# Optimization experiments

Measured on AMD Instinct MI355X. Metric: run time of the kernel, lower is better.

The kernel has to match this reference:

```python
import jax, jax.numpy as jnp
import numpy as np

N, S_CT, D = 64, 128, 1024
WIN = 5
EPS = 1e-8
STOP = 0.1
MAX_DEPTH = 25


def layer_norm(x, g, b, eps=1e-5):
    mu = jnp.mean(x, axis=-1, keepdims=True)
    var = jnp.var(x, axis=-1, keepdims=True)
    return (x - mu) / jnp.sqrt(var + eps) * g + b


def _augment(sequence, input_mask, START, END):
    n, s, d = sequence.shape
    seq = jnp.concatenate([jnp.broadcast_to(START, (n, 1, d)), sequence], axis=1)
    m = jnp.concatenate([jnp.ones((n, 1, 1), seq.dtype), input_mask], axis=1)
    m_no_end = jnp.concatenate([m, jnp.zeros((n, 1, 1), seq.dtype)], axis=1)
    m_yes_end = jnp.concatenate([jnp.ones((n, 1, 1), seq.dtype), m], axis=1)
    end_mask = m_yes_end - m_no_end  # one-hot at END slot
    seq = jnp.concatenate([seq, jnp.zeros((n, 1, d), seq.dtype)], axis=1)
    seq = end_mask * END + (1.0 - end_mask) * seq
    m_no_start = jnp.concatenate([jnp.zeros((n, 1, 1), seq.dtype), m_yes_end[:, 1:]], axis=1)
    return seq, m_yes_end, end_mask, m_no_start, m_no_end


def _neighbor_probs(exist_probs, mask):
    # exist_probs, mask: (n,s,1). Returns left/right soft-neighbor matrices (n,s,s).
    n, s, _ = mask.shape
    m = jnp.stack([mask[:, ::-1, 0], mask[:, :, 0]], axis=1)            # (n,2,s)
    p = jnp.stack([exist_probs[:, ::-1, 0], exist_probs[:, :, 0]], axis=1)
    tri = jnp.triu(jnp.ones((s, s), mask.dtype), k=1)
    mat = (p * m)[:, :, None, :] * tri                                   # (n,2,s,s)
    cs = jnp.cumsum(mat, axis=-1)
    rem_left = jnp.concatenate([jnp.ones((n, 2, s, 1), mask.dtype), 1.0 - cs[..., :-1]], axis=-1)
    rem_left = jnp.maximum(rem_left, 0.0)
    right = jnp.where(cs > 1.0, rem_left, mat) * m[:, :, None, :]
    left = jnp.flip(right[:, 0], axis=(1, 2))
    return left, right[:, 1]


def crvnn_forward(sequence, input_mask, START, END, W_conv, b_conv, W_scorer, b_scorer,
                  W_init, b_init, W_cell1, b_cell1, W_cell2, b_cell2,
                  ln1_g, ln1_b, ln2_g, ln2_b):
    seq, mask, end_mask, m_no_start, m_no_end = _augment(sequence, input_mask, START, END)
    n, s, d = seq.shape
    last_mask = jnp.concatenate([end_mask[:, 1:], jnp.zeros((n, 1, 1), seq.dtype)], axis=1)
    sel_mask = m_no_start * m_no_end * (1.0 - last_mask)  # start_end_last_mask
    seq = layer_norm((seq * mask) @ W_init + b_init, ln1_g, ln1_b) * mask
    exist = jnp.ones((n, s, 1), seq.dtype) * mask

    def step(carry, _):
        sq, ep, um = carry
        L, R = _neighbor_probs(ep, mask)
        l1 = L @ sq; l2 = L @ l1
        r1 = R @ sq; r2 = R @ r1
        win = jnp.concatenate([l2, l1, sq, r1, r2], axis=-1)  # (n,s,5d) == stacked window flattened
        h = jax.nn.gelu(win @ W_conv + b_conv, approximate=False)
        sc = h @ W_scorer + b_scorer                           # (n,s,1) transition score
        scores = jnp.concatenate([sc, jnp.zeros_like(sc)], axis=-1)
        exp_scores = jnp.exp(scores - jnp.max(scores))
        exp_t = exp_scores[..., 0:1] * sel_mask
        exp_n = exp_scores[..., 1:2]
        # sum_normalize over {transition, no_op}; gate halted samples via um (tp=0 => no-op)
        tp = exp_t / (exp_t + exp_n + 2.0 * EPS) * um[:, None, None]
        # compose(left_child, self)
        cat = jnp.concatenate([l1, sq], axis=-1)
        hid = jax.nn.gelu(cat @ W_cell1 + b_cell1, approximate=False)
        contents = (hid @ W_cell2 + b_cell2).reshape(n, s, 4, d)
        gates = jax.nn.sigmoid(contents[:, :, 0:3, :])
        comp = layer_norm(gates[:, :, 0] * l1 + gates[:, :, 1] * sq + gates[:, :, 2] * contents[:, :, 3, :], ln2_g, ln2_b)
        new_sq = tp * comp + (1.0 - tp) * sq
        new_ep = ep * (1.0 - (R @ tp))  # left neighbor consumed with prob of right neighbor transition
        active = jnp.sum(new_ep * sel_mask, axis=(1, 2))
        new_um = um * (active >= STOP).astype(sq.dtype)
        return (new_sq, new_ep, new_um), None

    steps = min(s - 2, MAX_DEPTH)
    (seq, exist, _), _ = jax.lax.scan(step, (seq, exist, jnp.ones((n,), seq.dtype)), None, length=steps)
    seq = seq * mask
    global_state = jnp.sum(last_mask * seq, axis=1)  # root lands at last content slot
    return seq[:, 1:-1, :], global_state


def setup_inputs():
    key = jax.random.key(0)
    ks = jax.random.split(key, 8)
    sc = 0.02
    f32 = jnp.float32
    return {
        "sequence": jax.random.normal(ks[0], (N, S_CT, D), f32),
        "input_mask": jnp.ones((N, S_CT, 1), f32),
        "START": jax.random.normal(ks[1], (D,), f32),
        "END": jax.random.normal(ks[2], (D,), f32),
        "W_conv": jax.random.normal(ks[3], (WIN * D, D), f32) * sc,
        "b_conv": jnp.zeros((D,), f32),
        "W_scorer": jax.random.normal(ks[4], (D, 1), f32) * sc,
        "b_scorer": jnp.zeros((1,), f32),
        "W_init": jax.random.normal(ks[5], (D, D), f32) * sc,
        "b_init": jnp.zeros((D,), f32),
        "W_cell1": jax.random.normal(ks[6], (2 * D, 4 * D), f32) * sc,
        "b_cell1": jnp.zeros((4 * D,), f32),
        "W_cell2": jax.random.normal(ks[7], (4 * D, 4 * D), f32) * sc,
        "b_cell2": jnp.zeros((4 * D,), f32),
        "ln1_g": jnp.ones((D,), f32), "ln1_b": jnp.zeros((D,), f32),
        "ln2_g": jnp.ones((D,), f32), "ln2_b": jnp.zeros((D,), f32),
    }


def reference(sequence, input_mask, START, END, W_conv, b_conv, W_scorer, b_scorer,
              W_init, b_init, W_cell1, b_cell1, W_cell2, b_cell2,
              ln1_g, ln1_b, ln2_g, ln2_b):
    return crvnn_forward(sequence, input_mask, START, END, W_conv, b_conv, W_scorer, b_scorer,
                         W_init, b_init, W_cell1, b_cell1, W_cell2, b_cell2,
                         ln1_g, ln1_b, ln2_g, ln2_b)
```

## Files before the change

kernel.cpp:

```cpp
#include <hip/hip_runtime.h>
#include <math.h>


#define NB 64
#define SS 130
#define DD 1024
#define MM (NB*SS)
#define LSTR 132
#define CROWS 1664
#define RSC 2048.0f
#define IRS (1.0f/2048.0f)

typedef _Float16 f16x8 __attribute__((ext_vector_type(8)));
typedef _Float16 f16x4 __attribute__((ext_vector_type(4)));
typedef _Float16 f16x2 __attribute__((ext_vector_type(2)));
typedef float f32x4 __attribute__((ext_vector_type(4)));

struct GemmSrcF { const float* a[5]; };
struct GemmSrcP { const _Float16* h[5]; const _Float16* l[5]; };
struct hl2 { _Float16 h, l; };

__device__ __forceinline__ float bsum(float v){
  __shared__ float sh[4];
  __syncthreads();
  #pragma unroll
  for (int o=32;o;o>>=1) v += __shfl_down(v,o);
  if ((threadIdx.x & 63)==0) sh[threadIdx.x>>6] = v;
  __syncthreads();
  return sh[0]+sh[1]+sh[2]+sh[3];
}
__device__ __forceinline__ float bmaxr(float v){
  __shared__ float sh[4];
  __syncthreads();
  #pragma unroll
  for (int o=32;o;o>>=1) v = fmaxf(v,__shfl_down(v,o));
  if ((threadIdx.x & 63)==0) sh[threadIdx.x>>6] = v;
  __syncthreads();
  return fmaxf(fmaxf(sh[0],sh[1]),fmaxf(sh[2],sh[3]));
}
__device__ __forceinline__ float gelu_(float x){
  return 0.5f*x*(1.f+erff(x*0.70710678118654752f));
}
__device__ __forceinline__ hl2 enc(float x){
  hl2 r;
  r.h = (_Float16)x;
  r.l = (_Float16)((x - (float)r.h)*RSC);
  return r;
}

__global__ __launch_bounds__(256) void build_masks(
    const float* __restrict__ im, float* __restrict__ mk, float* __restrict__ sel,
    float* __restrict__ lastm, float* __restrict__ endm, float* __restrict__ ep,
    float* __restrict__ um, int* __restrict__ flag){
  int b = blockIdx.x, i = threadIdx.x;
  if (i < SS){
    float mye = (i<=1) ? 1.f : im[b*128 + (i-2)];
    float mne = (i==SS-1) ? 0.f : ((i==0) ? 1.f : im[b*128 + (i-1)]);
    float em  = mye - mne;
    float mns = (i==0) ? 0.f : mye;
    float lm;
    if (i < SS-1){
      int i1 = i+1;
      float mye1 = (i1<=1) ? 1.f : im[b*128 + (i1-2)];
      float mne1 = (i1==SS-1) ? 0.f : im[b*128 + (i1-1)];
      lm = mye1 - mne1;
    } else lm = 0.f;
    float sl = mns * mne * (1.f - lm);
    int idx = b*SS + i;
    mk[idx]=mye; sel[idx]=sl; lastm[idx]=lm; endm[idx]=em; ep[idx]=mye;
  } else if (i == SS) { um[b] = 1.f; }
  else if (i == SS+1 && b==0) { flag[0] = 0; }
}

__global__ __launch_bounds__(256) void build_seq(
    const float* __restrict__ seqin, const float* __restrict__ START,
    const float* __restrict__ END, const float* __restrict__ mk,
    const float* __restrict__ endm, float* __restrict__ out){
  int r = blockIdx.x; int b = r/SS, i = r%SS; int t = threadIdx.x;
  float em = endm[r], m = mk[r];
  #pragma unroll
  for (int q=0;q<4;q++){
    int j = t + q*256;
    float v;
    if (i==0) v = START[j];
    else if (i<=128) v = seqin[((size_t)b*128 + (i-1))*DD + j];
    else v = 0.f;
    v = em*END[j] + (1.f-em)*v;
    out[(size_t)r*DD + j] = v*m;
  }
}

__global__ __launch_bounds__(256) void wtranspose(
    const float* __restrict__ W, _Float16* __restrict__ WTh, _Float16* __restrict__ WTl,
    int K, int N){
  __shared__ float Ts[32][33];
  int k0 = blockIdx.x*32, n0 = blockIdx.y*32;
  int t = threadIdx.x;
  int r = t>>3, c4 = (t&7)*4;
  float4 v = *(const float4*)(W + (size_t)(k0+r)*N + n0 + c4);
  Ts[r][c4]=v.x; Ts[r][c4+1]=v.y; Ts[r][c4+2]=v.z; Ts[r][c4+3]=v.w;
  __syncthreads();
  int n = t>>3, k4 = (t&7)*4;
  f16x4 h, lo;
  #pragma unroll
  for (int i=0;i<4;i++){
    hl2 e = enc(Ts[k4+i][n] * 64.f);
    h[i] = e.h; lo[i] = e.l;
  }
  *(f16x4*)(WTh + (size_t)(n0+n)*K + k0+k4) = h;
  *(f16x4*)(WTl + (size_t)(n0+n)*K + k0+k4) = lo;
}

template<bool PREW>
__global__ __launch_bounds__(256,2) void gemm_mfma(
    GemmSrcP S, long lda,
    const _Float16* __restrict__ WTh, const _Float16* __restrict__ WTl,
    const float* __restrict__ Wf, int Nw,
    const float* __restrict__ bias,
    float* __restrict__ C, _Float16* __restrict__ Ch, _Float16* __restrict__ Cl,
    long ldc, int K, int act,
    const int* __restrict__ flag, float* __restrict__ spart, const float* __restrict__ Ws){
  if (flag[0]) return;
  __shared__ _Float16 Ah[128][40], Al[128][40];
  __shared__ _Float16 Wh[128][40], Wl[128][40];
  const int t = threadIdx.x;
  const int wave = t >> 6, lane = t & 63;
  const int wm = wave >> 1, wn = wave & 1;
  const int l15 = lane & 15, l4 = lane >> 4;
  int lin = blockIdx.y * gridDim.x + blockIdx.x;
  int nwg = gridDim.x * gridDim.y;
  int q = nwg >> 3, r = nwg & 7;
  int xcd = lin & 7, pos = lin >> 3;
  int wg = (xcd < r) ? (xcd*(q+1) + pos) : (r*(q+1) + (xcd - r)*q + pos);
  int MT = gridDim.y;
  int mt = wg % MT, nt = wg / MT;
  const long mb = (long)mt * 128;
  const int  nb = nt * 128;
  f32x4 accH[4][4], accX[4][4];
  #pragma unroll
  for (int i=0;i<4;i++)
    #pragma unroll
    for (int j=0;j<4;j++){ accH[i][j] = (f32x4){0.f,0.f,0.f,0.f}; accX[i][j] = (f32x4){0.f,0.f,0.f,0.f}; }

  for (int kt=0; kt<K; kt+=32){
    #pragma unroll
    for (int p=0;p<2;p++){
      int f = t + 256*p;
      int m = f >> 2;
      int ko = (f & 3) * 8;
      int kg = kt + ko;
      const _Float16* sh = S.h[kg >> 10];
      const _Float16* sl = S.l[kg >> 10];
      *(f16x8*)&Ah[m][ko] = *(const f16x8*)(sh + (mb + m)*lda + (kg & 1023));
      *(f16x8*)&Al[m][ko] = *(const f16x8*)(sl + (mb + m)*lda + (kg & 1023));
    }
    if constexpr (PREW){
      #pragma unroll
      for (int p=0;p<2;p++){
        int f = t + 256*p;
        int n = f >> 2;
        int ko = (f & 3) * 8;
        *(f16x8*)&Wh[n][ko] = *(const f16x8*)(WTh + (size_t)(nb + n)*K + kt + ko);
        *(f16x8*)&Wl[n][ko] = *(const f16x8*)(WTl + (size_t)(nb + n)*K + kt + ko);
      }
    } else {
      #pragma unroll
      for (int p=0;p<2;p++){
        int u = t + 256*p;
        int kp = u >> 5;
        int c  = u & 31;
        const float* wsrc = Wf + (size_t)(kt + 2*kp)*Nw + nb + c;
        #pragma unroll
        for (int i=0;i<4;i++){
          hl2 e0 = enc(wsrc[32*i] * 64.f);
          hl2 e1 = enc(wsrc[(size_t)Nw + 32*i] * 64.f);
          f16x2 hp; hp[0]=e0.h; hp[1]=e1.h;
          f16x2 lp; lp[0]=e0.l; lp[1]=e1.l;
          int n = c + 32*i;
          *(f16x2*)&Wh[n][2*kp] = hp;
          *(f16x2*)&Wl[n][2*kp] = lp;
        }
      }
    }
    __syncthreads();
    f16x8 wh[4], wl[4];
    #pragma unroll
    for (int i=0;i<4;i++){
      wh[i] = *(const f16x8*)&Wh[wn*64 + i*16 + l15][8*l4];
      wl[i] = *(const f16x8*)&Wl[wn*64 + i*16 + l15][8*l4];
    }
    #pragma unroll
    for (int mi=0;mi<4;mi++){
      f16x8 ahv = *(const f16x8*)&Ah[wm*64 + mi*16 + l15][8*l4];
      f16x8 alv = *(const f16x8*)&Al[wm*64 + mi*16 + l15][8*l4];
      #pragma unroll
      for (int ni=0;ni<4;ni++){
        accH[mi][ni] = __builtin_amdgcn_mfma_f32_16x16x32_f16(wh[ni], ahv, accH[mi][ni], 0,0,0);
        accX[mi][ni] = __builtin_amdgcn_mfma_f32_16x16x32_f16(wh[ni], alv, accX[mi][ni], 0,0,0);
        accX[mi][ni] = __builtin_amdgcn_mfma_f32_16x16x32_f16(wl[ni], ahv, accX[mi][ni], 0,0,0);
      }
    }
    __syncthreads();
  }

  const float IH = 1.f/64.f, IX = 1.f/131072.f;
  if (act==2){
    #pragma unroll
    for (int mi=0;mi<4;mi++){
      float s = 0.f;
      #pragma unroll
      for (int ni=0;ni<4;ni++){
        int nbase = nb + wn*64 + ni*16 + 4*l4;
        #pragma unroll
        for (int rr=0;rr<4;rr++){
          float v = gelu_(accH[mi][ni][rr]*IH + accX[mi][ni][rr]*IX + bias[nbase+rr]);
          s = fmaf(v, Ws[nbase+rr], s);
        }
      }
      s += __shfl_xor(s, 16);
      s += __shfl_xor(s, 32);
      if (l4==0){
        long m = mb + wm*64 + mi*16 + l15;
        spart[m*16 + nt*2 + wn] = s;
      }
    }
    return;
  }
  #pragma unroll
  for (int mi=0;mi<4;mi++){
    long m = mb + wm*64 + mi*16 + l15;
    #pragma unroll
    for (int ni=0;ni<4;ni++){
      int nbase = nb + wn*64 + ni*16 + 4*l4;
      float v0 = accH[mi][ni][0]*IH + accX[mi][ni][0]*IX + bias[nbase+0];
      float v1 = accH[mi][ni][1]*IH + accX[mi][ni][1]*IX + bias[nbase+1];
      float v2 = accH[mi][ni][2]*IH + accX[mi][ni][2]*IX + bias[nbase+2];
      float v3 = accH[mi][ni][3]*IH + accX[mi][ni][3]*IX + bias[nbase+3];
      if (act==1){
        v0=gelu_(v0); v1=gelu_(v1); v2=gelu_(v2); v3=gelu_(v3);
        hl2 e0=enc(v0), e1=enc(v1), e2=enc(v2), e3=enc(v3);
        f16x4 h4; h4[0]=e0.h; h4[1]=e1.h; h4[2]=e2.h; h4[3]=e3.h;
        f16x4 l4v; l4v[0]=e0.l; l4v[1]=e1.l; l4v[2]=e2.l; l4v[3]=e3.l;
        *(f16x4*)(Ch + m*ldc + nbase) = h4;
        *(f16x4*)(Cl + m*ldc + nbase) = l4v;
      } else {
        float4 v; v.x=v0; v.y=v1; v.z=v2; v.w=v3;
        *(float4*)(C + m*ldc + nbase) = v;
      }
    }
  }
}

__global__ __launch_bounds__(256,2) void gemm_f32(
    GemmSrcF S, long lda, const float* __restrict__ B, const float* __restrict__ bias,
    float* __restrict__ C, long ldc, int N, int K, int act,
    const int* __restrict__ flag){
  if (flag[0]) return;
  __shared__ float Asm[16][132];
  __shared__ float Bsm[16][132];
  float acc[8][8];
  #pragma unroll
  for (int i=0;i<8;i++)
    #pragma unroll
    for (int j=0;j<8;j++) acc[i][j]=0.f;
  const int t = threadIdx.x;
  const int tx = t & 15, ty = t >> 4;
  const long mb = (long)blockIdx.y * 128;
  const int  nb = blockIdx.x * 128;
  for (int kt=0; kt<K; kt+=16){
    #pragma unroll
    for (int ii=0; ii<2; ii++){
      int f  = t + 256*ii;
      int m  = f >> 2;
      int k4 = (f & 3) * 4;
      int kg = kt + k4;
      const float* src = S.a[kg >> 10];
      float4 v = *(const float4*)(src + (mb + m)*lda + (kg & 1023));
      Asm[k4+0][m]=v.x; Asm[k4+1][m]=v.y; Asm[k4+2][m]=v.z; Asm[k4+3][m]=v.w;
    }
    #pragma unroll
    for (int ii=0; ii<2; ii++){
      int f  = t + 256*ii;
      int kk = f >> 5;
      int c4 = (f & 31)*4;
      *(float4*)&Bsm[kk][c4] = *(const float4*)(B + (long)(kt+kk)*N + nb + c4);
    }
    __syncthreads();
    #pragma unroll
    for (int kk=0;kk<16;kk++){
      float av[8], bv[8];
      *(float4*)&av[0] = *(const float4*)&Asm[kk][ty*4];
      *(float4*)&av[4] = *(const float4*)&Asm[kk][64+ty*4];
      *(float4*)&bv[0] = *(const float4*)&Bsm[kk][tx*4];
      *(float4*)&bv[4] = *(const float4*)&Bsm[kk][64+tx*4];
      #pragma unroll
      for (int r=0;r<8;r++)
        #pragma unroll
        for (int c=0;c<8;c++) acc[r][c] = fmaf(av[r],bv[c],acc[r][c]);
    }
    __syncthreads();
  }
  #pragma unroll
  for (int rh=0;rh<2;rh++)
  #pragma unroll
  for (int rr=0;rr<4;rr++){
    long row = mb + rh*64 + ty*4 + rr;
    #pragma unroll
    for (int ch=0;ch<2;ch++){
      int col = nb + ch*64 + tx*4;
      float4 v;
      v.x = acc[rh*4+rr][ch*4+0] + bias[col+0];
      v.y = acc[rh*4+rr][ch*4+1] + bias[col+1];
      v.z = acc[rh*4+rr][ch*4+2] + bias[col+2];
      v.w = acc[rh*4+rr][ch*4+3] + bias[col+3];
      *(float4*)(C + row*ldc + col) = v;
    }
  }
}

__global__ __launch_bounds__(256,2) void bgemm(
    const float* __restrict__ P,
    const _Float16* __restrict__ Xh, const _Float16* __restrict__ Xl,
    _Float16* __restrict__ Yh, _Float16* __restrict__ Yl,
    const int* __restrict__ flag){
  if (flag[0]) return;
  __shared__ float Ps[64][17];
  __shared__ float Xs[16][132];
  const int t = threadIdx.x;
  const int nt = blockIdx.x, mt = blockIdx.y, b = blockIdx.z;
  const int i0 = mt*64;
  const float* Pb = P + (size_t)b*SS*LSTR;
  const _Float16* Xhb = Xh + (size_t)b*SS*DD + nt*128;
  const _Float16* Xlb = Xl + (size_t)b*SS*DD + nt*128;
  _Float16* Yhb = Yh + (size_t)b*SS*DD + nt*128;
  _Float16* Ylb = Yl + (size_t)b*SS*DD + nt*128;
  const int tx = t & 7, ty = t >> 3;
  float acc[2][16];
  #pragma unroll
  for (int r=0;r<2;r++)
    #pragma unroll
    for (int c=0;c<16;c++) acc[r][c]=0.f;
  for (int j0=0;j0<SS;j0+=16){
    { int r = t>>2, c0 = (t&3)*4;
      float4 v = make_float4(0.f,0.f,0.f,0.f);
      if (i0 + r < SS && j0 + c0 < LSTR) v = *(const float4*)(Pb + (size_t)(i0+r)*LSTR + j0 + c0);
      Ps[r][c0]=v.x; Ps[r][c0+1]=v.y; Ps[r][c0+2]=v.z; Ps[r][c0+3]=v.w;
    }
    #pragma unroll
    for (int ii=0;ii<2;ii++){
      int f = t + 256*ii;
      int jj = f>>5, c4 = (f&31)*4;
      float x0=0.f,x1=0.f,x2=0.f,x3=0.f;
      if (j0 + jj < SS){
        f16x4 xh = *(const f16x4*)(Xhb + (size_t)(j0+jj)*DD + c4);
        f16x4 xl = *(const f16x4*)(Xlb + (size_t)(j0+jj)*DD + c4);
        x0 = (float)xh[0] + (float)xl[0]*IRS;
        x1 = (float)xh[1] + (float)xl[1]*IRS;
        x2 = (float)xh[2] + (float)xl[2]*IRS;
        x3 = (float)xh[3] + (float)xl[3]*IRS;
      }
      Xs[jj][c4]=x0; Xs[jj][c4+1]=x1; Xs[jj][c4+2]=x2; Xs[jj][c4+3]=x3;
    }
    __syncthreads();
    #pragma unroll
    for (int jj=0;jj<16;jj++){
      float p0 = Ps[2*ty][jj], p1 = Ps[2*ty+1][jj];
      #pragma unroll
      for (int q=0;q<4;q++){
        float4 xv = *(const float4*)&Xs[jj][tx*4 + 32*q];
        acc[0][q*4+0] = fmaf(p0,xv.x,acc[0][q*4+0]);
        acc[0][q*4+1] = fmaf(p0,xv.y,acc[0][q*4+1]);
        acc[0][q*4+2] = fmaf(p0,xv.z,acc[0][q*4+2]);
        acc[0][q*4+3] = fmaf(p0,xv.w,acc[0][q*4+3]);
        acc[1][q*4+0] = fmaf(p1,xv.x,acc[1][q*4+0]);
        acc[1][q*4+1] = fmaf(p1,xv.y,acc[1][q*4+1]);
        acc[1][q*4+2] = fmaf(p1,xv.z,acc[1][q*4+2]);
        acc[1][q*4+3] = fmaf(p1,xv.w,acc[1][q*4+3]);
      }
    }
    __syncthreads();
  }
  #pragma unroll
  for (int rr=0;rr<2;rr++){
    int row = i0 + 2*ty + rr;
    if (row < SS){
      #pragma unroll
      for (int q=0;q<4;q++){
        hl2 e0 = enc(acc[rr][q*4+0]);
        hl2 e1 = enc(acc[rr][q*4+1]);
        hl2 e2 = enc(acc[rr][q*4+2]);
        hl2 e3 = enc(acc[rr][q*4+3]);
        f16x4 h4; h4[0]=e0.h; h4[1]=e1.h; h4[2]=e2.h; h4[3]=e3.h;
        f16x4 l4v; l4v[0]=e0.l; l4v[1]=e1.l; l4v[2]=e2.l; l4v[3]=e3.l;
        *(f16x4*)(Yhb + (size_t)row*DD + tx*4 + 32*q) = h4;
        *(f16x4*)(Ylb + (size_t)row*DD + tx*4 + 32*q) = l4v;
      }
    }
  }
}

__global__ __launch_bounds__(256) void neighbor_kernel(
    const float* __restrict__ ep, const float* __restrict__ mk,
    float* __restrict__ L, float* __restrict__ R, const int* __restrict__ flag){
  if (flag[0]) return;
  int wave = threadIdx.x >> 6, lane = threadIdx.x & 63;
  int idx = blockIdx.x*4 + wave;
  if (idx >= MM) return;
  int b = idx / SS, i = idx % SS;
  const float* p = ep + b*SS;
  const float* m = mk + b*SS;
  float mR[3], mL[3], mv[3];
  #pragma unroll
  for (int c=0;c<3;c++){
    int j = lane + 64*c;
    float pj = (j<SS)? p[j] : 0.f;
    float mj = (j<SS)? m[j] : 0.f;
    mv[c] = mj;
    float x = pj*mj;
    mR[c] = (j>i)? x : 0.f;
    mL[c] = (j<i)? x : 0.f;
  }
  float csR[3]; float run = 0.f;
  #pragma unroll
  for (int c=0;c<3;c++){
    float s = mR[c];
    #pragma unroll
    for (int o=1;o<64;o<<=1){ float v = __shfl_up(s,o); if (lane>=o) s += v; }
    csR[c] = s + run;
    run += __shfl(s,63);
  }
  float csL[3]; run = 0.f;
  #pragma unroll
  for (int cc=0;cc<3;cc++){
    int c = 2-cc;
    float s = mL[c];
    #pragma unroll
    for (int o=1;o<64;o<<=1){ float v = __shfl_down(s,o); if (lane < 64-o) s += v; }
    csL[c] = s + run;
    run += __shfl(s,0);
  }
  float* Lr = L + (size_t)idx*LSTR;
  float* Rr = R + (size_t)idx*LSTR;
  #pragma unroll
  for (int c=0;c<3;c++){
    int j = lane + 64*c;
    if (j < LSTR){
      float rv = 0.f, lv = 0.f;
      if (j < SS){
        rv = ((csR[c]>1.f) ? fmaxf(1.f-(csR[c]-mR[c]),0.f) : mR[c]) * mv[c];
        lv = ((csL[c]>1.f) ? fmaxf(1.f-(csL[c]-mL[c]),0.f) : mL[c]) * mv[c];
      }
      Rr[j] = rv; Lr[j] = lv;
    }
  }
}

__global__ __launch_bounds__(256) void ln1_kernel(
    const float* __restrict__ xin, const float* __restrict__ g, const float* __restrict__ bb,
    const float* __restrict__ mk, _Float16* __restrict__ sqh, _Float16* __restrict__ sql){
  int r = blockIdx.x, t = threadIdx.x;
  const float* xr = xin + (size_t)r*DD;
  float x[4]; float s=0.f;
  #pragma unroll
  for (int q=0;q<4;q++){ x[q]=xr[t+256*q]; s+=x[q]; }
  float mean = bsum(s)*(1.f/DD);
  float vs=0.f;
  #pragma unroll
  for (int q=0;q<4;q++){ float d=x[q]-mean; vs+=d*d; }
  float var = bsum(vs)*(1.f/DD);
  float inv = 1.f/sqrtf(var+1e-5f);
  float m = mk[r];
  #pragma unroll
  for (int q=0;q<4;q++){
    int j=t+256*q;
    float v = ((x[q]-mean)*inv*g[j]+bb[j])*m;
    hl2 e = enc(v);
    sqh[(size_t)r*DD+j] = e.h; sql[(size_t)r*DD+j] = e.l;
  }
}

__global__ void scorer_final(const float* __restrict__ spart, const float* __restrict__ bs,
                             float* __restrict__ sc, const int* __restrict__ flag){
  if (flag[0]) return;
  int r = blockIdx.x*blockDim.x + threadIdx.x;
  if (r >= MM) return;
  float s = bs[0];
  #pragma unroll
  for (int k=0;k<16;k++) s += spart[(size_t)r*16+k];
  sc[r] = s;
}
__global__ __launch_bounds__(256) void max1(const float* __restrict__ sc, float* __restrict__ part,
                                            const int* __restrict__ flag){
  if (flag[0]) return;
  int idx = blockIdx.x*256 + threadIdx.x;
  float v = -1e30f;
  for (int i = idx; i < MM; i += 64*256) v = fmaxf(v, sc[i]);
  v = bmaxr(v);
  if (threadIdx.x==0) part[blockIdx.x] = v;
}
__global__ __launch_bounds__(64) void max2(const float* __restrict__ part, float* __restrict__ gm,
                                           const int* __restrict__ flag){
  if (flag[0]) return;
  float v = part[threadIdx.x];
  #pragma unroll
  for (int o=32;o;o>>=1) v = fmaxf(v, __shfl_down(v,o));
  if (threadIdx.x==0) gm[0] = fmaxf(v, 0.f);
}
__global__ void tp_kernel(const float* __restrict__ sc, const float* __restrict__ sel,
                          const float* __restrict__ um, const float* __restrict__ gm,
                          float* __restrict__ tp, const int* __restrict__ flag){
  if (flag[0]) return;
  int idx = blockIdx.x*blockDim.x + threadIdx.x;
  if (idx>=MM) return;
  int b = idx / SS;
  float g = gm[0];
  float et = expf(sc[idx]-g)*sel[idx];
  float en = expf(-g);
  tp[idx] = et/(et+en+2e-8f)*um[b];
}

__global__ __launch_bounds__(256) void update_kernel(
    const float* __restrict__ cont,
    const _Float16* __restrict__ l1h, const _Float16* __restrict__ l1l,
    _Float16* __restrict__ sqh, _Float16* __restrict__ sql,
    const float* __restrict__ tp, const float* __restrict__ g, const float* __restrict__ bb,
    const int* __restrict__ flag, long row0){
  if (flag[0]) return;
  long r = row0 + blockIdx.x; int t = threadIdx.x;
  const float* cr = cont + (size_t)blockIdx.x*4096;
  const _Float16* lh = l1h + (size_t)r*DD;
  const _Float16* ll = l1l + (size_t)r*DD;
  _Float16* sh = sqh + (size_t)r*DD;
  _Float16* sl = sql + (size_t)r*DD;
  float x[4], sv[4];
  float s=0.f;
  #pragma unroll
  for (int q=0;q<4;q++){
    int j = t+q*256;
    float c0=cr[j], c1=cr[DD+j], c2=cr[2*DD+j], c3=cr[3*DD+j];
    float g0=1.f/(1.f+expf(-c0));
    float g1=1.f/(1.f+expf(-c1));
    float g2=1.f/(1.f+expf(-c2));
    float lv = (float)lh[j] + (float)ll[j]*IRS;
    float sqv = (float)sh[j] + (float)sl[j]*IRS;
    sv[q]=sqv;
    x[q] = g0*lv + g1*sqv + g2*c3;
    s += x[q];
  }
  float mean = bsum(s)*(1.f/DD);
  float vs=0.f;
  #pragma unroll
  for (int q=0;q<4;q++){ float d=x[q]-mean; vs+=d*d; }
  float var = bsum(vs)*(1.f/DD);
  float inv = 1.f/sqrtf(var+1e-5f);
  float tpv = tp[r];
  #pragma unroll
  for (int q=0;q<4;q++){
    int j=t+q*256;
    float comp = (x[q]-mean)*inv*g[j]+bb[j];
    float out = tpv*comp + (1.f-tpv)*sv[q];
    hl2 e = enc(out);
    sh[j]=e.h; sl[j]=e.l;
  }
}

__global__ __launch_bounds__(256) void ep_update(
    float* __restrict__ ep, const float* __restrict__ R,
    const float* __restrict__ tp, const int* __restrict__ flag){
  if (flag[0]) return;
  int wave = threadIdx.x >> 6, lane = threadIdx.x & 63;
  int idx = blockIdx.x*4 + wave;
  if (idx >= MM) return;
  int b = idx / SS;
  const float* Rr = R + (size_t)idx*LSTR;
  const float* tb = tp + b*SS;
  float d = 0.f;
  #pragma unroll
  for (int c=0;c<3;c++){
    int j = lane + 64*c;
    if (j < SS) d = fmaf(Rr[j], tb[j], d);
  }
  #pragma unroll
  for (int o=32;o;o>>=1) d += __shfl_xor(d,o);
  if (lane==0) ep[idx] *= (1.f - d);
}

__global__ __launch_bounds__(256) void active_um(const float* __restrict__ ep,
                                                 const float* __restrict__ sel,
                                                 float* __restrict__ um,
                                                 const int* __restrict__ flag){
  if (flag[0]) return;
  int b = blockIdx.x, t = threadIdx.x;
  float s = (t<SS) ? ep[b*SS+t]*sel[b*SS+t] : 0.f;
  s = bsum(s);
  if (t==0) um[b] *= (s >= 0.1f) ? 1.f : 0.f;
}
__global__ __launch_bounds__(64) void done_kernel(const float* __restrict__ um, int* __restrict__ flag){
  float v = um[threadIdx.x];
  unsigned long long b = __ballot(v > 0.f);
  if (threadIdx.x==0) flag[0] = (b==0ULL) ? 1 : 0;
}

__global__ __launch_bounds__(256) void output_kernel(
    const _Float16* __restrict__ sqh, const _Float16* __restrict__ sql,
    const float* __restrict__ mk, float* __restrict__ out){
  int r = blockIdx.x; int b = r/SS, i = r%SS;
  if (i<1 || i>128) return;
  float m = mk[r]; int t=threadIdx.x;
  #pragma unroll
  for (int q=0;q<4;q++){
    int j = t+q*256;
    float v = (float)sqh[(size_t)r*DD+j] + (float)sql[(size_t)r*DD+j]*IRS;
    out[((size_t)b*128 + (i-1))*DD + j] = v*m;
  }
}
__global__ __launch_bounds__(256) void gstate_kernel(
    const _Float16* __restrict__ sqh, const _Float16* __restrict__ sql,
    const float* __restrict__ mk, const float* __restrict__ lastm,
    float* __restrict__ outg){
  int b = blockIdx.x; int t=threadIdx.x;
  #pragma unroll
  for (int q=0;q<4;q++){
    int j = t+q*256;
    float acc=0.f;
    for (int i=0;i<SS;i++){
      float w = lastm[b*SS+i]*mk[b*SS+i];
      size_t o = ((size_t)(b*SS+i))*DD + j;
      float v = (float)sqh[o] + (float)sql[o]*IRS;
      acc = fmaf(w, v, acc);
    }
    outg[(size_t)b*DD + j] = acc;
  }
}

extern "C" void kernel_launch(void* const* d_in, const int* in_sizes, int n_in,
                              void* d_out, int out_size, void* d_ws, size_t ws_size,
                              hipStream_t stream) {
  const float* sequence   = (const float*)d_in[0];
  const float* input_mask = (const float*)d_in[1];
  const float* START      = (const float*)d_in[2];
  const float* END        = (const float*)d_in[3];
  const float* W_conv     = (const float*)d_in[4];
  const float* b_conv     = (const float*)d_in[5];
  const float* W_scorer   = (const float*)d_in[6];
  const float* b_scorer   = (const float*)d_in[7];
  const float* W_init     = (const float*)d_in[8];
  const float* b_init     = (const float*)d_in[9];
  const float* W_cell1    = (const float*)d_in[10];
  const float* b_cell1    = (const float*)d_in[11];
  const float* W_cell2    = (const float*)d_in[12];
  const float* b_cell2    = (const float*)d_in[13];
  const float* ln1g       = (const float*)d_in[14];
  const float* ln1b       = (const float*)d_in[15];
  const float* ln2g       = (const float*)d_in[16];
  const float* ln2b       = (const float*)d_in[17];

  float* ws = (float*)d_ws;
  const size_t U = (size_t)MM*DD;
  _Float16* sq_h = (_Float16*)(ws);        _Float16* sq_l = sq_h + U;
  _Float16* l1_h = (_Float16*)(ws + U);    _Float16* l1_l = l1_h + U;
  _Float16* r1_h = (_Float16*)(ws + 2*U);  _Float16* r1_l = r1_h + U;
  _Float16* l2_h = (_Float16*)(ws + 3*U);  _Float16* l2_l = l2_h + U;
  _Float16* r2_h = (_Float16*)(ws + 4*U);  _Float16* r2_l = r2_h + U;
  float* contb = ws + 4*U;
  float* seqtmp  = ws + U;
  float* inittmp = ws + 2*U;
  float* Lm   = ws + 5*U;
  float* Rm   = Lm + (size_t)NB*SS*LSTR;
  float* maskv= Rm + (size_t)NB*SS*LSTR;
  float* sel  = maskv + MM;
  float* lastm= sel + MM;
  float* endm = lastm + MM;
  float* ep   = endm + MM;
  float* scb  = ep + MM;
  float* tpb  = scb + MM;
  float* spart= tpb + MM;
  float* umb  = spart + (size_t)MM*16;
  float* part = umb + NB;
  float* gmx  = part + 64;
  int*   flag = (int*)(gmx + 4);
  size_t used_floats = (size_t)((float*)(flag+4) - ws);
  used_floats = (used_floats + 7) & ~(size_t)7;
  const size_t SC = (size_t)1024*5120, S1 = (size_t)4096*2048, S2 = (size_t)4096*4096;
  _Float16* WT2_h = (_Float16*)(ws + used_floats);
  _Float16* WT2_l = WT2_h + S2;
  _Float16* WT1_h = WT2_l + S2;
  _Float16* WT1_l = WT1_h + S1;
  _Float16* WTc_h = WT1_l + S1;
  _Float16* WTc_l = WTc_h + SC;
  const bool pre2 = ws_size >= (size_t)((char*)(WT2_l + S2) - (char*)d_ws);
  const bool pre1 = ws_size >= (size_t)((char*)(WT1_l + S1) - (char*)d_ws);
  const bool prec = ws_size >= (size_t)((char*)(WTc_l + SC) - (char*)d_ws);

  build_masks<<<NB,256,0,stream>>>(input_mask, maskv, sel, lastm, endm, ep, umb, flag);
  build_seq<<<MM,256,0,stream>>>(sequence, START, END, maskv, endm, seqtmp);
  GemmSrcF si; si.a[0]=seqtmp; si.a[1]=seqtmp; si.a[2]=seqtmp; si.a[3]=seqtmp; si.a[4]=seqtmp;
  gemm_f32<<<dim3(8,65),256,0,stream>>>(si, DD, W_init, b_init, inittmp, DD, DD, DD, 0, flag);
  ln1_kernel<<<MM,256,0,stream>>>(inittmp, ln1g, ln1b, maskv, sq_h, sq_l);

  if (pre2) wtranspose<<<dim3(128,128),256,0,stream>>>(W_cell2, WT2_h, WT2_l, 4096, 4096);
  if (pre1) wtranspose<<<dim3(64,128),256,0,stream>>>(W_cell1, WT1_h, WT1_l, 2048, 4096);
  if (prec) wtranspose<<<dim3(160,32),256,0,stream>>>(W_conv,  WTc_h, WTc_l, 5120, 1024);

  const int NBLK = (MM + 3) / 4;
  for (int it=0; it<25; ++it){
    neighbor_kernel<<<NBLK,256,0,stream>>>(ep, maskv, Lm, Rm, flag);
    bgemm<<<dim3(8,3,NB),256,0,stream>>>(Lm, sq_h, sq_l, l1_h, l1_l, flag);
    bgemm<<<dim3(8,3,NB),256,0,stream>>>(Rm, sq_h, sq_l, r1_h, r1_l, flag);
    bgemm<<<dim3(8,3,NB),256,0,stream>>>(Lm, l1_h, l1_l, l2_h, l2_l, flag);
    bgemm<<<dim3(8,3,NB),256,0,stream>>>(Rm, r1_h, r1_l, r2_h, r2_l, flag);
    GemmSrcP s5;
    s5.h[0]=l2_h; s5.h[1]=l1_h; s5.h[2]=sq_h; s5.h[3]=r1_h; s5.h[4]=r2_h;
    s5.l[0]=l2_l; s5.l[1]=l1_l; s5.l[2]=sq_l; s5.l[3]=r1_l; s5.l[4]=r2_l;
    if (prec)
      gemm_mfma<true ><<<dim3(8,65),256,0,stream>>>(s5, DD, WTc_h, WTc_l, nullptr, 0, b_conv, nullptr, nullptr, nullptr, 0, 5120, 2, flag, spart, W_scorer);
    else
      gemm_mfma<false><<<dim3(8,65),256,0,stream>>>(s5, DD, nullptr, nullptr, W_conv, 1024, b_conv, nullptr, nullptr, nullptr, 0, 5120, 2, flag, spart, W_scorer);
    scorer_final<<<(MM+255)/256,256,0,stream>>>(spart, b_scorer, scb, flag);
    max1<<<64,256,0,stream>>>(scb, part, flag);
    max2<<<1,64,0,stream>>>(part, gmx, flag);
    tp_kernel<<<(MM+255)/256,256,0,stream>>>(scb, sel, umb, gmx, tpb, flag);
    for (int c=0;c<5;c++){
      long row0 = (long)c*CROWS;
      GemmSrcP s2;
      s2.h[0]=l1_h+row0*DD; s2.h[1]=sq_h+row0*DD; s2.h[2]=s2.h[1]; s2.h[3]=s2.h[1]; s2.h[4]=s2.h[1];
      s2.l[0]=l1_l+row0*DD; s2.l[1]=sq_l+row0*DD; s2.l[2]=s2.l[1]; s2.l[3]=s2.l[1]; s2.l[4]=s2.l[1];
      GemmSrcP s3;
      s3.h[0]=l2_h; s3.h[1]=l2_h+DD; s3.h[2]=l2_h+2*DD; s3.h[3]=l2_h+3*DD; s3.h[4]=l2_h;
      s3.l[0]=l2_l; s3.l[1]=l2_l+DD; s3.l[2]=l2_l+2*DD; s3.l[3]=l2_l+3*DD; s3.l[4]=l2_l;
      if (pre1)
        gemm_mfma<true ><<<dim3(32,13),256,0,stream>>>(s2, DD,   WT1_h, WT1_l, nullptr, 0, b_cell1, nullptr, l2_h, l2_l, 4096, 2048, 1, flag, nullptr, nullptr);
      else
        gemm_mfma<false><<<dim3(32,13),256,0,stream>>>(s2, DD,   nullptr, nullptr, W_cell1, 4096, b_cell1, nullptr, l2_h, l2_l, 4096, 2048, 1, flag, nullptr, nullptr);
      if (pre2)
        gemm_mfma<true ><<<dim3(32,13),256,0,stream>>>(s3, 4096, WT2_h, WT2_l, nullptr, 0, b_cell2, contb, nullptr, nullptr, 4096, 4096, 0, flag, nullptr, nullptr);
      else
        gemm_mfma<false><<<dim3(32,13),256,0,stream>>>(s3, 4096, nullptr, nullptr, W_cell2, 4096, b_cell2, contb, nullptr, nullptr, 4096, 4096, 0, flag, nullptr, nullptr);
      update_kernel<<<CROWS,256,0,stream>>>(contb, l1_h, l1_l, sq_h, sq_l, tpb, ln2g, ln2b, flag, row0);
    }
    ep_update<<<NBLK,256,0,stream>>>(ep, Rm, tpb, flag);
    active_um<<<NB,256,0,stream>>>(ep, sel, umb, flag);
    done_kernel<<<1,64,0,stream>>>(umb, flag);
  }

  float* out = (float*)d_out;
  output_kernel<<<MM,256,0,stream>>>(sq_h, sq_l, maskv, out);
  gstate_kernel<<<NB,256,0,stream>>>(sq_h, sq_l, maskv, lastm, out + (size_t)NB*128*DD);
}
```

Baseline: 63.81 ms.

## Load GEMM tiles directly into LDS with XOR-swizzled unpadded layout

Replaces register-staged global-to-shared copies of the A and pre-transposed W tiles with direct global_load_lds 16-byte transfers. The padded 40-wide rows become a 32-wide layout with an XOR swizzle on the 8-element chunk index to avoid bank conflicts. The fp32-weight path is also rewritten so each thread converts 8 consecutive k values into one swizzled chunk. The aim is to cut VGPR pressure and instruction overhead in the load phase, at the cost of strided global reads in the unpacked-weight path and correctness risk from the layout mapping of the direct LDS loads.

```diff
diff --git a/kernel.cpp b/kernel.cpp
--- a/kernel.cpp
+++ b/kernel.cpp
@@ -13,12 +13,18 @@
 
 typedef _Float16 f16x8 __attribute__((ext_vector_type(8)));
 typedef _Float16 f16x4 __attribute__((ext_vector_type(4)));
-typedef _Float16 f16x2 __attribute__((ext_vector_type(2)));
 typedef float f32x4 __attribute__((ext_vector_type(4)));
 
 struct GemmSrcF { const float* a[5]; };
 struct GemmSrcP { const _Float16* h[5]; const _Float16* l[5]; };
 struct hl2 { _Float16 h, l; };
+
+typedef const __attribute__((address_space(1))) void* gas_ptr;
+typedef __attribute__((address_space(3))) void* las_ptr;
+
+__device__ __forceinline__ void gload16(const void* g, void* l){
+  __builtin_amdgcn_global_load_lds((gas_ptr)g, (las_ptr)l, 16, 0, 0);
+}
 
 __device__ __forceinline__ float bsum(float v){
   __shared__ float sh[4];
@@ -121,8 +127,8 @@
     long ldc, int K, int act,
     const int* __restrict__ flag, float* __restrict__ spart, const float* __restrict__ Ws){
   if (flag[0]) return;
-  __shared__ _Float16 Ah[128][40], Al[128][40];
-  __shared__ _Float16 Wh[128][40], Wl[128][40];
+  __shared__ _Float16 Ah[128*32], Al[128*32];
+  __shared__ _Float16 Wh[128*32], Wl[128*32];
   const int t = threadIdx.x;
   const int wave = t >> 6, lane = t & 63;
   const int wm = wave >> 1, wn = wave & 1;
@@ -147,52 +153,61 @@
     for (int p=0;p<2;p++){
       int f = t + 256*p;
       int m = f >> 2;
-      int ko = (f & 3) * 8;
-      int kg = kt + ko;
+      int qs = f & 3;
+      int qd = qs ^ (m & 3);
+      int kg = kt + qd*8;
       const _Float16* sh = S.h[kg >> 10];
       const _Float16* sl = S.l[kg >> 10];
-      *(f16x8*)&Ah[m][ko] = *(const f16x8*)(sh + (mb + m)*lda + (kg & 1023));
-      *(f16x8*)&Al[m][ko] = *(const f16x8*)(sl + (mb + m)*lda + (kg & 1023));
+      size_t goff = (size_t)(mb + m)*lda + (kg & 1023);
+      int lbase = (wave*64 + 256*p)*8;
+      gload16(sh + goff, &Ah[lbase]);
+      gload16(sl + goff, &Al[lbase]);
     }
     if constexpr (PREW){
       #pragma unroll
       for (int p=0;p<2;p++){
         int f = t + 256*p;
         int n = f >> 2;
-        int ko = (f & 3) * 8;
-        *(f16x8*)&Wh[n][ko] = *(const f16x8*)(WTh + (size_t)(nb + n)*K + kt + ko);
-        *(f16x8*)&Wl[n][ko] = *(const f16x8*)(WTl + (size_t)(nb + n)*K + kt + ko);
+        int qs = f & 3;
+        int qd = qs ^ (n & 3);
+        size_t goff = (size_t)(nb + n)*K + kt + qd*8;
+        int lbase = (wave*64 + 256*p)*8;
+        gload16(WTh + goff, &Wh[lbase]);
+        gload16(WTl + goff, &Wl[lbase]);
       }
     } else {
       #pragma unroll
       for (int p=0;p<2;p++){
-        int u = t + 256*p;
-        int kp = u >> 5;
-        int c  = u & 31;
-        const float* wsrc = Wf + (size_t)(kt + 2*kp)*Nw + nb + c;
+        int idx = t + 256*p;
+        int n = idx >> 2;
+        int qs = idx & 3;
+        int qd = qs ^ (n & 3);
+        const float* wsrc = Wf + (size_t)(kt + qd*8)*Nw + nb + n;
+        f16x8 h8, l8;
         #pragma unroll
-        for (int i=0;i<4;i++){
-          hl2 e0 = enc(wsrc[32*i] * 64.f);
-          hl2 e1 = enc(wsrc[(size_t)Nw + 32*i] * 64.f);
-          f16x2 hp; hp[0]=e0.h; hp[1]=e1.h;
-          f16x2 lp; lp[0]=e0.l; lp[1]=e1.l;
-          int n = c + 32*i;
-          *(f16x2*)&Wh[n][2*kp] = hp;
-          *(f16x2*)&Wl[n][2*kp] = lp;
+        for (int j=0;j<8;j++){
+          hl2 e = enc(wsrc[(size_t)j*Nw] * 64.f);
+          h8[j]=e.h; l8[j]=e.l;
         }
+        *(f16x8*)&Wh[idx*8] = h8;
+        *(f16x8*)&Wl[idx*8] = l8;
       }
     }
     __syncthreads();
     f16x8 wh[4], wl[4];
     #pragma unroll
     for (int i=0;i<4;i++){
-      wh[i] = *(const f16x8*)&Wh[wn*64 + i*16 + l15][8*l4];
-      wl[i] = *(const f16x8*)&Wl[wn*64 + i*16 + l15][8*l4];
+      int rw = wn*64 + i*16 + l15;
+      int off = rw*32 + (l4 ^ (rw&3))*8;
+      wh[i] = *(const f16x8*)&Wh[off];
+      wl[i] = *(const f16x8*)&Wl[off];
     }
     #pragma unroll
     for (int mi=0;mi<4;mi++){
-      f16x8 ahv = *(const f16x8*)&Ah[wm*64 + mi*16 + l15][8*l4];
-      f16x8 alv = *(const f16x8*)&Al[wm*64 + mi*16 + l15][8*l4];
+      int ra = wm*64 + mi*16 + l15;
+      int off = ra*32 + (l4 ^ (ra&3))*8;
+      f16x8 ahv = *(const f16x8*)&Ah[off];
+      f16x8 alv = *(const f16x8*)&Al[off];
       #pragma unroll
       for (int ni=0;ni<4;ni++){
         accH[mi][ni] = __builtin_amdgcn_mfma_f32_16x16x32_f16(wh[ni], ahv, accH[mi][ni], 0,0,0);
```

Measured after the change: 79.50 ms. 24.6% more time.
